# Kernel optimization log

Hardware: AMD Instinct MI355X
Metric: run time of the kernel (lower is better)

Reference implementation:

```python
import jax, jax.numpy as jnp
import numpy as np

H, KVH, D, R = 32, 8, 128, 32
MASK_OUT = 0.5
NEG = -1e9  # stand-in for finfo.min to avoid -inf accumulation; preserves ordering/softmax
ROPE_THETA = 10000.0


def _rope_tables(S, D):
    inv = 1.0 / (ROPE_THETA ** (np.arange(0, D, 2, dtype=np.float32) / D))
    t = np.arange(S, dtype=np.float32)
    freqs = np.outer(t, inv)
    emb = np.concatenate([freqs, freqs], axis=-1)  # [S, D]
    return jnp.asarray(np.cos(emb)), jnp.asarray(np.sin(emb))


def _apply_rope(x, cos, sin):
    # x: [B,H,S,D]; cos/sin: [S,D]
    x1, x2 = jnp.split(x, 2, axis=-1)
    rot = jnp.concatenate([-x2, x1], axis=-1)
    return x * cos[None, None] + rot * sin[None, None]


def setup_inputs() -> dict:
    B, S, E = 1, 1024, 4096
    key = jax.random.key(0)
    ks = jax.random.split(key, 9)
    n = lambda k, shp, sc=0.02: jax.random.normal(k, shp, jnp.float32) * sc
    return {
        'hidden_states': n(ks[0], (B, S, E), 1.0),
        'wq': n(ks[1], (E, H * D)),
        'wk': n(ks[2], (E, KVH * D)),
        'wv': n(ks[3], (E, KVH * D)),
        'wo': n(ks[4], (H * D, E)),
        'mixq': n(ks[5], (E, R)),
        'mixk': n(ks[6], (E, R)),
        'q_pos': n(ks[7], (S, H, R, D)),
        'k_pos': n(ks[8], (S, H, R, D)),
    }


def reference(hidden_states, wq, wk, wv, wo, mixq, mixk, q_pos, k_pos):
    B, S, E = hidden_states.shape
    rep = H // KVH
    # QKV projections -> [B, heads, S, D]
    q = (hidden_states @ wq).reshape(B, S, H, D).transpose(0, 2, 1, 3)
    k = (hidden_states @ wk).reshape(B, S, KVH, D).transpose(0, 2, 1, 3)
    v = (hidden_states @ wv).reshape(B, S, KVH, D).transpose(0, 2, 1, 3)
    k = jnp.repeat(k, rep, axis=1)  # repeat_kv (GQA expand) -> [B,H,S,D]
    v = jnp.repeat(v, rep, axis=1)

    cos, sin = _rope_tables(S, D)
    qr = _apply_rope(q, cos, sin)
    kr = _apply_rope(k, cos, sin)
    scale = 1.0 / jnp.sqrt(jnp.float32(D))
    true_score = jnp.einsum('bhqd,bhkd->bhqk', qr, kr) * scale  # [B,H,S,S]

    # low-rank position-dependent draft score
    lrq = hidden_states @ mixq  # [B,S,R]
    lrk = hidden_states @ mixk
    pq = jnp.einsum('bmr,mhrd->bhmd', lrq, q_pos)  # [B,H,S,D]
    pk = jnp.einsum('bnr,nhrd->bhnd', lrk, k_pos)
    draft_score = jnp.einsum('bhqd,bhkd->bhqk', pq, pk)  # [B,H,S,S]

    causal = jnp.where(jnp.tril(jnp.ones((S, S), dtype=bool)), 0.0, NEG).astype(jnp.float32)[None, None]
    draft_score = draft_score + causal  # prefill: add causal mask to draft score

    num_remain = S - int(S * MASK_OUT)
    _, draft_idx = jax.lax.top_k(draft_score, num_remain)  # [B,H,S,K]

    # scatter 0 at kept kv positions, NEG elsewhere
    bi = jnp.arange(B)[:, None, None, None]
    hi = jnp.arange(H)[None, :, None, None]
    qi = jnp.arange(S)[None, None, :, None]
    topk_mask = jnp.full((B, H, S, S), NEG, jnp.float32).at[bi, hi, qi, draft_idx].set(0.0)

    probs = jax.nn.softmax(true_score + causal + topk_mask, axis=-1)
    out = jnp.einsum('bhqk,bhkd->bqhd', probs, v).reshape(B, S, H * D)
    return out @ wo
```

## Files before the change

kernel.cpp:

```cpp
#include <hip/hip_runtime.h>
#include <hip/hip_bf16.h>
#include <math.h>


typedef unsigned short u16;
typedef unsigned long long u64;
using bf16x8 = __attribute__((ext_vector_type(8))) short;
using f32x4  = __attribute__((ext_vector_type(4))) float;

#define NEGBIG -1e30f
#define QSCALE 0.08838834764831845f

__device__ __forceinline__ unsigned int fkey(float f) {
    unsigned int u = __float_as_uint(f);
    return (u & 0x80000000u) ? ~u : (u | 0x80000000u);
}

__device__ __forceinline__ u16 f2b(float f) {
    union { float f; unsigned u; } x; x.f = f;
    unsigned r = x.u + 0x7fffu + ((x.u >> 16) & 1u);
    return (u16)(r >> 16);
}

__device__ __forceinline__ void gl_lds16(const u16* g, u16* l) {
    __builtin_amdgcn_global_load_lds(
        (__attribute__((address_space(1))) void*)(g),
        (__attribute__((address_space(3))) void*)(l), 16, 0, 0);
}

__device__ __forceinline__ void rope_table_calc(int row, int i,
    float* __restrict__ cosb, float* __restrict__ sinb)
{
    double inv = pow(10000.0, -((double)(2 * i)) / 128.0);
    double ang = (double)row * inv;
    cosb[row * 64 + i] = (float)cos(ang);
    sinb[row * 64 + i] = (float)sin(ang);
}

__device__ __forceinline__ void transpose_tile(
    const float* __restrict__ in, u16* __restrict__ out, int Kdim, int N,
    int bx, int by)
{
    __shared__ u16 tile[64][66];
    int n0 = bx * 64, k0 = by * 64;
    int t = threadIdx.x;
#pragma unroll
    for (int u = 0; u < 16; ++u) {
        int e = u * 256 + t; int r = e >> 6, c = e & 63;
        tile[r][c] = f2b(in[(size_t)(k0 + r) * N + n0 + c]);
    }
    __syncthreads();
#pragma unroll
    for (int u = 0; u < 16; ++u) {
        int e = u * 256 + t; int r = e >> 6, c = e & 63;
        out[(size_t)(n0 + r) * Kdim + k0 + c] = tile[c][r];
    }
}

__global__ __launch_bounds__(256) void transpose_bf16_kernel(
    const float* __restrict__ in, u16* __restrict__ out, int Kdim, int N)
{
    transpose_tile(in, out, Kdim, N, blockIdx.x, blockIdx.y);
}

__global__ __launch_bounds__(256) void init_kernel(
    const float* __restrict__ hs, u16* __restrict__ hs_bf,
    float* __restrict__ cosb, float* __restrict__ sinb)
{
    int bx = blockIdx.x, t = threadIdx.x;
    if (bx < 4096) {
        int i = bx * 256 + t;
        float4 v = ((const float4*)hs)[i];
        u16 o[4] = {f2b(v.x), f2b(v.y), f2b(v.z), f2b(v.w)};
        ((uint2*)hs_bf)[i] = *(const uint2*)o;
    } else {
        rope_table_calc((bx - 4096) * 4 + (t >> 6), t & 63, cosb, sinb);
    }
}

__global__ __launch_bounds__(256) void transpose_qkvw_kernel(
    const float* __restrict__ wq, const float* __restrict__ wk, const float* __restrict__ wv,
    u16* __restrict__ wqT, u16* __restrict__ wkT, u16* __restrict__ wvT)
{
    int bx = blockIdx.x;
    const float* in; u16* outp; int N;
    if (bx < 64)      { in = wq; outp = wqT; N = 4096; }
    else if (bx < 80) { in = wk; outp = wkT; N = 1024; bx -= 64; }
    else              { in = wv; outp = wvT; N = 1024; bx -= 80; }
    transpose_tile(in, outp, 4096, N, bx, blockIdx.y);
}

__global__ __launch_bounds__(128) void rope_pack2_kernel(
    const float* __restrict__ qb, const float* __restrict__ kb,
    const float* __restrict__ cosb, const float* __restrict__ sinb,
    u16* __restrict__ qr, u16* __restrict__ kr)
{
    int s = blockIdx.x, h = blockIdx.y, d = threadIdx.x;
    const float* src; u16* dst; int W; float scale;
    if (h < 32) { src = qb; dst = qr; W = 4096; scale = QSCALE; }
    else        { h -= 32; src = kb; dst = kr; W = 1024; scale = 1.0f; }
    float x  = src[(size_t)s * W + h * 128 + d];
    float x2 = src[(size_t)s * W + h * 128 + (d ^ 64)];
    float cs = cosb[s * 64 + (d & 63)];
    float sn = sinb[s * 64 + (d & 63)];
    float rot = (d < 64) ? -x2 : x2;
    dst[((size_t)h * 1024 + s) * 128 + d] = f2b((x * cs + rot * sn) * scale);
}

__global__ __launch_bounds__(256) void lr_kernel(
    const float* __restrict__ hs, const float* __restrict__ mixq, const float* __restrict__ mixk,
    float* __restrict__ lrq, float* __restrict__ lrk)
{
    __shared__ float row[4096];
    __shared__ float part[2][32][4];
    int m = blockIdx.x, t = threadIdx.x;
#pragma unroll
    for (int u = 0; u < 4; ++u)
        ((float4*)row)[t + u * 256] = ((const float4*)(hs + (size_t)m * 4096))[t + u * 256];
    __syncthreads();
    int r = t & 31, which = (t >> 5) & 1, quarter = t >> 6;
    const float* mix = which ? mixk : mixq;
    float acc = 0.f;
    int kbase = quarter * 1024;
#pragma unroll 8
    for (int kk = 0; kk < 1024; ++kk)
        acc = fmaf(row[kbase + kk], mix[(size_t)(kbase + kk) * 32 + r], acc);
    part[which][r][quarter] = acc;
    __syncthreads();
    if (t < 64) {
        int r2 = t & 31, w2 = t >> 5;
        float s = part[w2][r2][0] + part[w2][r2][1] + part[w2][r2][2] + part[w2][r2][3];
        (w2 ? lrk : lrq)[(size_t)m * 32 + r2] = s;
    }
}

__global__ __launch_bounds__(128) void ppos2_kernel(
    const float* __restrict__ lrq, const float* __restrict__ lrk,
    const float* __restrict__ qpos, const float* __restrict__ kpos,
    float* __restrict__ pq, float* __restrict__ pk)
{
    int h = blockIdx.x, by = blockIdx.y, d = threadIdx.x;
    const float* lr; const float* pos; float* outp; int m;
    if (by < 512) { m = 512 + by; lr = lrq; pos = qpos; outp = pq; }
    else          { m = by - 512; lr = lrk; pos = kpos; outp = pk; }
    __shared__ float lrs[32];
    if (d < 32) lrs[d] = lr[(size_t)m * 32 + d];
    __syncthreads();
    const float* base = pos + ((size_t)(m * 32 + h) * 32) * 128 + d;
    float acc = 0.f;
#pragma unroll
    for (int r = 0; r < 32; ++r)
        acc = fmaf(lrs[r], base[(size_t)r * 128], acc);
    outp[((size_t)h * 1024 + m) * 128 + d] = acc;
}

__global__ __launch_bounds__(256) void init_fused_kernel(
    const float* __restrict__ hs, u16* __restrict__ hs_bf,
    float* __restrict__ cosb, float* __restrict__ sinb,
    const float* __restrict__ mixq, const float* __restrict__ mixk,
    float* __restrict__ lrq, float* __restrict__ lrk,
    const float* __restrict__ wq, const float* __restrict__ wk, const float* __restrict__ wv,
    u16* __restrict__ wqT, u16* __restrict__ wkT, u16* __restrict__ wvT)
{
    __shared__ float row[4096];
    __shared__ float part[2][32][4];
    int bx = blockIdx.x, t = threadIdx.x;
    if (bx < 4096) {
        int i = bx * 256 + t;
        float4 v = ((const float4*)hs)[i];
        u16 o[4] = {f2b(v.x), f2b(v.y), f2b(v.z), f2b(v.w)};
        ((uint2*)hs_bf)[i] = *(const uint2*)o;
    } else if (bx < 4352) {
        rope_table_calc((bx - 4096) * 4 + (t >> 6), t & 63, cosb, sinb);
    } else if (bx < 5376) {
        int m = bx - 4352;
#pragma unroll
        for (int u = 0; u < 4; ++u)
            ((float4*)row)[t + u * 256] = ((const float4*)(hs + (size_t)m * 4096))[t + u * 256];
        __syncthreads();
        int r = t & 31, which = (t >> 5) & 1, quarter = t >> 6;
        const float* mix = which ? mixk : mixq;
        float acc = 0.f;
        int kbase = quarter * 1024;
#pragma unroll 8
        for (int kk = 0; kk < 1024; ++kk)
            acc = fmaf(row[kbase + kk], mix[(size_t)(kbase + kk) * 32 + r], acc);
        part[which][r][quarter] = acc;
        __syncthreads();
        if (t < 64) {
            int r2 = t & 31, w2 = t >> 5;
            float s = part[w2][r2][0] + part[w2][r2][1] + part[w2][r2][2] + part[w2][r2][3];
            (w2 ? lrk : lrq)[(size_t)m * 32 + r2] = s;
        }
    } else {
        int idx = bx - 5376;
        int bxT = idx % 96, byT = idx / 96;
        const float* in; u16* outp; int N;
        if (bxT < 64)      { in = wq; outp = wqT; N = 4096; }
        else if (bxT < 80) { in = wk; outp = wkT; N = 1024; bxT -= 64; }
        else               { in = wv; outp = wvT; N = 1024; bxT -= 80; }
        transpose_tile(in, outp, 4096, N, bxT, byT);
    }
}

__device__ __forceinline__ void gemm_bf16_panel(
    const u16* __restrict__ Ap, const u16* __restrict__ Bp,
    float* __restrict__ Cp, int Kdim, int kbase, int klen, int Cst)
{
    __shared__ u16 As[128 * 32];
    __shared__ u16 Bs[128 * 32];
    const int t = threadIdx.x;
    const int wave = t >> 6, lane = t & 63;
    const int wr = wave >> 1, wc = wave & 1;
    const int fr = lane & 15, fq = lane >> 4;

    f32x4 acc[4][4];
#pragma unroll
    for (int m = 0; m < 4; ++m)
#pragma unroll
        for (int n = 0; n < 4; ++n) acc[m][n] = 0.f;

    const int srow = 32 * wave + (lane >> 2);
    const int skc = (lane & 3) * 8;
    const u16* aS = Ap + (size_t)srow * Kdim + kbase + skc;
    const u16* bS = Bp + (size_t)srow * Kdim + kbase + skc;
    u16* aD0 = As + 1024 * wave;  u16* aD1 = aD0 + 512;
    u16* bD0 = Bs + 1024 * wave;  u16* bD1 = bD0 + 512;

    const int aoff = (wr * 64 + fr) * 32 + fq * 8;
    const int boff = (wc * 64 + fr) * 32 + fq * 8;

    for (int k0 = 0; k0 < klen; k0 += 32) {
        __syncthreads();
        gl_lds16(aS + k0, aD0);
        gl_lds16(aS + (size_t)16 * Kdim + k0, aD1);
        gl_lds16(bS + k0, bD0);
        gl_lds16(bS + (size_t)16 * Kdim + k0, bD1);
        __syncthreads();

        bf16x8 af[4], bfr[4];
#pragma unroll
        for (int m = 0; m < 4; ++m) af[m] = *(const bf16x8*)(As + aoff + m * 512);
#pragma unroll
        for (int n = 0; n < 4; ++n) bfr[n] = *(const bf16x8*)(Bs + boff + n * 512);
#pragma unroll
        for (int m = 0; m < 4; ++m)
#pragma unroll
            for (int n = 0; n < 4; ++n)
                acc[m][n] = __builtin_amdgcn_mfma_f32_16x16x32_bf16(af[m], bfr[n], acc[m][n], 0, 0, 0);
    }

    float* Cb = Cp + (size_t)(wr * 64 + fq * 4) * Cst + wc * 64 + fr;
#pragma unroll
    for (int m = 0; m < 4; ++m)
#pragma unroll
        for (int j = 0; j < 4; ++j)
#pragma unroll
            for (int n = 0; n < 4; ++n)
                Cb[(size_t)(m * 16 + j) * Cst + n * 16] = acc[m][n][j];
}

__global__ __launch_bounds__(256) void gemm_qkv_bf16_kernel(
    const u16* __restrict__ hs_bf, const u16* __restrict__ wqT,
    const u16* __restrict__ wkT, const u16* __restrict__ wvT,
    float* __restrict__ q, float* __restrict__ k, float* __restrict__ v)
{
    int bn = blockIdx.x, bm = blockIdx.y;
    const u16* Bsel; float* Csel; int Ncols;
    if (bn < 32)      { Bsel = wqT; Csel = q; Ncols = 4096; }
    else if (bn < 40) { Bsel = wkT; Csel = k; Ncols = 1024; bn -= 32; }
    else              { Bsel = wvT; Csel = v; Ncols = 1024; bn -= 40; }
    gemm_bf16_panel(hs_bf + (size_t)bm * 128 * 4096, Bsel + (size_t)bn * 128 * 4096,
                    Csel + (size_t)bm * 128 * Ncols + bn * 128, 4096, 0, 4096, Ncols);
}

__global__ __launch_bounds__(256) void gemm_wo_bf16_kernel(
    const u16* __restrict__ attn_bf, const u16* __restrict__ woT, float* __restrict__ out)
{
    int bn = blockIdx.x, bm = blockIdx.y;
    gemm_bf16_panel(attn_bf + (size_t)bm * 128 * 4096, woT + (size_t)bn * 128 * 4096,
                    out + (size_t)bm * 128 * 4096 + bn * 128, 4096, 0, 4096, 4096);
}

__global__ __launch_bounds__(256) void qkv_ppos_kernel(
    const u16* __restrict__ hs_bf, const u16* __restrict__ wqT,
    const u16* __restrict__ wkT, const u16* __restrict__ wvT,
    float* __restrict__ C,
    const float* __restrict__ lrq, const float* __restrict__ lrk,
    const float* __restrict__ qpos, const float* __restrict__ kpos,
    float* __restrict__ pq, float* __restrict__ pk)
{
    int bx = blockIdx.x, t = threadIdx.x;
    if (bx < 384) {
        int bn = bx % 48, bm = bx / 48;
        const u16* Bsel; int bnrow;
        if (bn < 32)      { Bsel = wqT; bnrow = bn; }
        else if (bn < 40) { Bsel = wkT; bnrow = bn - 32; }
        else              { Bsel = wvT; bnrow = bn - 40; }
        gemm_bf16_panel(hs_bf + (size_t)bm * 128 * 4096, Bsel + (size_t)bnrow * 128 * 4096,
                        C + (size_t)bm * 128 * 6144 + bn * 128, 4096, 0, 4096, 6144);
    } else {
        int idx = bx - 384;
        int bp = idx >> 5, h = idx & 31;
        int sub = t >> 7, d = t & 127;
        int by = bp * 2 + sub;
        const float* lr; const float* pos; float* outp; int m;
        if (by < 512) { m = 512 + by; lr = lrq; pos = qpos; outp = pq; }
        else          { m = by - 512; lr = lrk; pos = kpos; outp = pk; }
        __shared__ float lrs[2][32];
        if (d < 32) lrs[sub][d] = lr[(size_t)m * 32 + d];
        __syncthreads();
        const float* base = pos + ((size_t)(m * 32 + h) * 32) * 128 + d;
        float acc = 0.f;
#pragma unroll
        for (int r = 0; r < 32; ++r)
            acc = fmaf(lrs[sub][r], base[(size_t)r * 128], acc);
        outp[((size_t)h * 1024 + m) * 128 + d] = acc;
    }
}

__device__ __forceinline__ void reduce_rope_item(
    const float* __restrict__ C,
    const float* __restrict__ cosb, const float* __restrict__ sinb,
    u16* __restrict__ qr, u16* __restrict__ kr, int bx)
{
    int t = threadIdx.x;
    int sp = bx & 511, h40 = bx >> 9;
    int s = sp * 2 + (t >> 7), d = t & 127;
    int col; u16* dst; float scale;
    if (h40 < 32) { col = h40 * 128 + d; dst = qr + ((size_t)h40 * 1024 + s) * 128 + d; scale = QSCALE; }
    else { col = 4096 + (h40 - 32) * 128 + d; dst = kr + ((size_t)(h40 - 32) * 1024 + s) * 128 + d; scale = 1.0f; }
    int colp = col ^ 64;
    float x  = C[(size_t)s * 6144 + col];
    float x2 = C[(size_t)s * 6144 + colp];
    float cs = cosb[s * 64 + (d & 63)];
    float sn = sinb[s * 64 + (d & 63)];
    float rot = (d < 64) ? -x2 : x2;
    *dst = f2b((x * cs + rot * sn) * scale);
}

__device__ __forceinline__ void v_transpose_dev(
    const float* __restrict__ C, u16* __restrict__ vT, int idx)
{
    __shared__ u16 vtile[64][66];
    int bxT = idx & 15, byT = idx >> 4;
    int n0 = bxT * 64, k0 = byT * 64;
    int t = threadIdx.x;
#pragma unroll
    for (int u = 0; u < 16; ++u) {
        int e = u * 256 + t; int r = e >> 6, c = e & 63;
        vtile[r][c] = f2b(C[(size_t)(k0 + r) * 6144 + 5120 + n0 + c]);
    }
    __syncthreads();
#pragma unroll
    for (int u = 0; u < 16; ++u) {
        int e = u * 256 + t; int r = e >> 6, c = e & 63;
        vT[(size_t)(n0 + r) * 1024 + k0 + c] = vtile[c][r];
    }
}

__device__ __forceinline__ void draft_tile_compute(
    const float* __restrict__ pq, const float* __restrict__ pk,
    float* __restrict__ scores, int h0, int idx, int hh)
{
    int bm, bc;
    if (idx < 10)      { bm = 4; bc = idx; }
    else if (idx < 22) { bm = 5; bc = idx - 10; }
    else if (idx < 36) { bm = 6; bc = idx - 22; }
    else               { bm = 7; bc = idx - 36; }

    const float* A  = pq + ((size_t)(h0 + hh) * 1024 + bm * 128) * 128;
    const float* BT = pk + ((size_t)(h0 + hh) * 1024 + bc * 64) * 128;
    float* Cs = scores + ((size_t)hh * 512 + (bm - 4) * 128) * 1024 + bc * 64;

    __shared__ float As[8][128];
    __shared__ float Bs[8][64];
    const int t = threadIdx.x;
    const int tx = t & 15, ty = (t >> 4) & 15;

    float acc[8][4];
#pragma unroll
    for (int u = 0; u < 8; ++u)
#pragma unroll
        for (int w = 0; w < 4; ++w) acc[u][w] = 0.f;

    const int ai = t >> 1, ah = (t & 1) * 4;
    const int bi = t >> 2, bh = (t & 3) * 2;
    const float* Ap = A + (size_t)ai * 128 + ah;
    const float* Bp = BT + (size_t)bi * 128 + bh;

    for (int k0 = 0; k0 < 128; k0 += 8) {
        float4 av = *(const float4*)(Ap + k0);
        float2 bv = *(const float2*)(Bp + k0);
        __syncthreads();
        As[ah + 0][ai] = av.x; As[ah + 1][ai] = av.y;
        As[ah + 2][ai] = av.z; As[ah + 3][ai] = av.w;
        Bs[bh][bi] = bv.x; Bs[bh + 1][bi] = bv.y;
        __syncthreads();
#pragma unroll
        for (int kk = 0; kk < 8; ++kk) {
            float4 a0 = *(const float4*)(&As[kk][ty * 4]);
            float4 a1 = *(const float4*)(&As[kk][64 + ty * 4]);
            float4 b0 = *(const float4*)(&Bs[kk][tx * 4]);
            float aa[8] = {a0.x, a0.y, a0.z, a0.w, a1.x, a1.y, a1.z, a1.w};
#pragma unroll
            for (int u = 0; u < 8; ++u) {
                acc[u][0] = fmaf(aa[u], b0.x, acc[u][0]);
                acc[u][1] = fmaf(aa[u], b0.y, acc[u][1]);
                acc[u][2] = fmaf(aa[u], b0.z, acc[u][2]);
                acc[u][3] = fmaf(aa[u], b0.w, acc[u][3]);
            }
        }
    }
#pragma unroll
    for (int u = 0; u < 8; ++u) {
        int row = (u < 4) ? (ty * 4 + u) : (64 + ty * 4 + (u - 4));
        *(float4*)(Cs + (size_t)row * 1024 + tx * 4)
            = make_float4(acc[u][0], acc[u][1], acc[u][2], acc[u][3]);
    }
}

__global__ __launch_bounds__(256) void draft_gemm_kernel(
    const float* __restrict__ pq, const float* __restrict__ pk,
    float* __restrict__ scores, int h0)
{
    draft_tile_compute(pq, pk, scores, h0, blockIdx.x, blockIdx.y);
}

__global__ __launch_bounds__(256) void draft0_fused_kernel(
    const float* __restrict__ pq, const float* __restrict__ pk,
    float* __restrict__ scores, const float* __restrict__ C,
    const float* __restrict__ cosb, const float* __restrict__ sinb,
    u16* __restrict__ qr, u16* __restrict__ kr, u16* __restrict__ vT)
{
    int bx = blockIdx.x;
    if (bx < 416) draft_tile_compute(pq, pk, scores, 0, bx % 52, bx / 52);
    else if (bx < 416 + 20480) reduce_rope_item(C, cosb, sinb, qr, kr, bx - 416);
    else v_transpose_dev(C, vT, bx - 416 - 20480);
}

__global__ __launch_bounds__(256) void draft1_fused_kernel(
    const float* __restrict__ pq, const float* __restrict__ pk,
    float* __restrict__ scores, const float* __restrict__ wo, u16* __restrict__ woT)
{
    int bx = blockIdx.x;
    if (bx < 416) draft_tile_compute(pq, pk, scores, 8, bx % 52, bx / 52);
    else { int i = bx - 416; transpose_tile(wo, woT, 4096, 4096, i & 63, i >> 6); }
}

__global__ __launch_bounds__(256) void topk_select_kernel(
    const float* __restrict__ scores, int h0,
    unsigned long long* __restrict__ mask)
{
    int qt = blockIdx.x, hh = blockIdx.y;
    int h = h0 + hh;
    int t = threadIdx.x;
    const int i = t >> 4, jj = t & 15;
    const int lrow = qt * 16 + i;
    const int qrow = 512 + lrow;

    const float* src = scores + ((size_t)hh * 512 + lrow) * 1024;

    unsigned int vals[64];
#pragma unroll
    for (int g = 0; g < 16; ++g) {
        float4 v = *(const float4*)(src + g * 64 + jj * 4);
        int col = g * 64 + jj * 4;
        vals[g * 4 + 0] = fkey((col + 0) <= qrow ? v.x : NEGBIG);
        vals[g * 4 + 1] = fkey((col + 1) <= qrow ? v.y : NEGBIG);
        vals[g * 4 + 2] = fkey((col + 2) <= qrow ? v.z : NEGBIG);
        vals[g * 4 + 3] = fkey((col + 3) <= qrow ? v.w : NEGBIG);
    }

    unsigned int p = 0u;
    int kth = 512;
    for (int b = 31; b >= 0; --b) {
        unsigned int bit = 1u << b;
        unsigned int himask = (b == 31) ? 0u : (0xFFFFFFFFu << (b + 1));
        int cnt = 0;
#pragma unroll
        for (int n = 0; n < 64; ++n)
            cnt += (int)((((vals[n] ^ p) & himask) == 0u) && ((vals[n] & bit) != 0u));
        cnt += __shfl_xor(cnt, 1);
        cnt += __shfl_xor(cnt, 2);
        cnt += __shfl_xor(cnt, 4);
        cnt += __shfl_xor(cnt, 8);
        if (cnt >= kth) p |= bit; else kth -= cnt;
    }

    unsigned long long wpart[16];
#pragma unroll
    for (int w = 0; w < 16; ++w) wpart[w] = 0ull;
#pragma unroll
    for (int g = 0; g < 16; ++g)
#pragma unroll
        for (int e = 0; e < 4; ++e)
            wpart[g] |= ((unsigned long long)(vals[g * 4 + e] >= p)) << (4 * jj + e);
#pragma unroll
    for (int s = 1; s < 16; s <<= 1) {
#pragma unroll
        for (int w = 0; w < 16; ++w)
            wpart[w] |= __shfl_xor(wpart[w], s);
    }
    mask[((size_t)h * 1024 + qrow) * 16 + jj] = wpart[jj];
}

__global__ __launch_bounds__(256) void gemm_wo_sk_kernel(
    const u16* __restrict__ attn_bf, const u16* __restrict__ woT,
    float* __restrict__ D0, float* __restrict__ D1)
{
    int bn = blockIdx.x, bm = blockIdx.y, g = blockIdx.z;
    float* C = g ? D1 : D0;
    gemm_bf16_panel(attn_bf + (size_t)bm * 128 * 4096, woT + (size_t)bn * 128 * 4096,
                    C + (size_t)bm * 128 * 4096 + bn * 128, 4096, g * 2048, 2048, 4096);
}

__global__ __launch_bounds__(256) void reduce_out_kernel(
    const float* __restrict__ D0, const float* __restrict__ D1, float* __restrict__ out)
{
    int i = blockIdx.x * 256 + threadIdx.x;
    float4 a = ((const float4*)D0)[i];
    float4 b = ((const float4*)D1)[i];
    ((float4*)out)[i] = make_float4(a.x + b.x, a.y + b.y, a.z + b.z, a.w + b.w);
}

#define ATTN_KP 136
#define ATTN_VP 72

__global__ __launch_bounds__(256) void attn_mfma_kernel(
    const u16* __restrict__ qr, const u16* __restrict__ kr,
    const u16* __restrict__ vT,
    const unsigned long long* __restrict__ mask,
    u16* __restrict__ attn)
{
    int bx = blockIdx.x;
    int qt = (bx & 1) ? (bx >> 1) : (15 - (bx >> 1));
    int h = blockIdx.y;
    int kvh = h >> 2;
    int q0 = qt * 64;
    int t = threadIdx.x;
    int wave = t >> 6, lane = t & 63;
    int fr = lane & 15, fq = lane >> 4;
    int qrow = q0 + wave * 16 + fr;

    __shared__ u16 Ks[64 * ATTN_KP];
    __shared__ u16 Vs[128 * ATTN_VP];

    bf16x8 qf[4];
    const u16* qbase = qr + ((size_t)h * 1024 + qrow) * 128 + fq * 8;
#pragma unroll
    for (int kc = 0; kc < 4; ++kc)
        qf[kc] = *(const bf16x8*)(qbase + kc * 32);

    float m_run = -3.0e38f, l_run = 0.f;
    f32x4 accO[8];
#pragma unroll
    for (int m2 = 0; m2 < 8; ++m2) accO[m2] = 0.f;

    const unsigned long long* mrow = mask + ((size_t)h * 1024 + qrow) * 16;
    const bool use_mask = (qrow >= 512);
    const u16* kgh = kr + (size_t)kvh * 1024 * 128;
    const u16* vgh = vT + (size_t)kvh * 128 * 1024;

    int ntiles = qt + 1;
    for (int c = 0; c < ntiles; ++c) {
        int kv0 = c * 64;
        __syncthreads();
#pragma unroll
        for (int u = 0; u < 4; ++u) {
            int e = t + u * 256;
            int row = e >> 4, bc2 = (e & 15) * 8;
            uint4 d4 = *(const uint4*)(kgh + ((size_t)(kv0 + row)) * 128 + bc2);
            *(uint4*)(&Ks[row * ATTN_KP + bc2]) = d4;
        }
#pragma unroll
        for (int u = 0; u < 4; ++u) {
            int e = t + u * 256;
            int row = e >> 3, bc2 = (e & 7) * 8;
            uint4 d4 = *(const uint4*)(vgh + (size_t)row * 1024 + kv0 + bc2);
            *(uint4*)(&Vs[row * ATTN_VP + bc2]) = d4;
        }
        __syncthreads();

        f32x4 accS[4];
        accS[0] = 0.f; accS[1] = 0.f; accS[2] = 0.f; accS[3] = 0.f;
#pragma unroll
        for (int t2 = 0; t2 < 4; ++t2)
#pragma unroll
            for (int kc = 0; kc < 4; ++kc) {
                bf16x8 kf = *(const bf16x8*)(&Ks[(t2 * 16 + fr) * ATTN_KP + kc * 32 + fq * 8]);
                accS[t2] = __builtin_amdgcn_mfma_f32_16x16x32_bf16(kf, qf[kc], accS[t2], 0, 0, 0);
            }

        unsigned long long mw = use_mask ? mrow[c] : ~0ull;
        float p[4][4];
        float tmax = -3.0e38f;
#pragma unroll
        for (int t2 = 0; t2 < 4; ++t2)
#pragma unroll
            for (int j = 0; j < 4; ++j) {
                int kvi = (t2 << 4) + (fq << 2) + j;
                bool ok = ((mw >> kvi) & 1ull) && (kv0 + kvi <= qrow);
                float s = ok ? accS[t2][j] : -3.0e38f;
                p[t2][j] = s;
                tmax = fmaxf(tmax, s);
            }
        tmax = fmaxf(tmax, __shfl_xor(tmax, 16));
        tmax = fmaxf(tmax, __shfl_xor(tmax, 32));
        float m_new = fmaxf(m_run, tmax);
        float sf = __expf(m_run - m_new);
        float psum = 0.f;
#pragma unroll
        for (int t2 = 0; t2 < 4; ++t2)
#pragma unroll
            for (int j = 0; j < 4; ++j) {
                float e = (p[t2][j] > -1.0e38f) ? __expf(p[t2][j] - m_new) : 0.f;
                p[t2][j] = e;
                psum += e;
            }
        psum += __shfl_xor(psum, 16);
        psum += __shfl_xor(psum, 32);
        l_run = l_run * sf + psum;
        m_run = m_new;

#pragma unroll
        for (int m2 = 0; m2 < 8; ++m2) accO[m2] *= sf;

        union { uint4 u; bf16x8 b; } pc[2];
        int srcA = fr + ((fq & 1) << 5);
        int srcB = srcA + 16;
        bool hi = (fq & 2) != 0;
#pragma unroll
        for (int half = 0; half < 2; ++half) {
            unsigned W0, W1, W2, W3;
            asm("v_cvt_pk_bf16_f32 %0, %1, %2" : "=v"(W0) : "v"(p[2 * half][0]),     "v"(p[2 * half][1]));
            asm("v_cvt_pk_bf16_f32 %0, %1, %2" : "=v"(W1) : "v"(p[2 * half][2]),     "v"(p[2 * half][3]));
            asm("v_cvt_pk_bf16_f32 %0, %1, %2" : "=v"(W2) : "v"(p[2 * half + 1][0]), "v"(p[2 * half + 1][1]));
            asm("v_cvt_pk_bf16_f32 %0, %1, %2" : "=v"(W3) : "v"(p[2 * half + 1][2]), "v"(p[2 * half + 1][3]));
            unsigned a0 = __shfl(W0, srcA), a1 = __shfl(W1, srcA);
            unsigned a2 = __shfl(W2, srcA), a3 = __shfl(W3, srcA);
            unsigned b0 = __shfl(W0, srcB), b1 = __shfl(W1, srcB);
            unsigned b2 = __shfl(W2, srcB), b3 = __shfl(W3, srcB);
            pc[half].u.x = hi ? a2 : a0;
            pc[half].u.y = hi ? a3 : a1;
            pc[half].u.z = hi ? b2 : b0;
            pc[half].u.w = hi ? b3 : b1;
        }

#pragma unroll
        for (int m2 = 0; m2 < 8; ++m2) {
            bf16x8 vf0 = *(const bf16x8*)(&Vs[(m2 * 16 + fr) * ATTN_VP + fq * 8]);
            accO[m2] = __builtin_amdgcn_mfma_f32_16x16x32_bf16(vf0, pc[0].b, accO[m2], 0, 0, 0);
            bf16x8 vf1 = *(const bf16x8*)(&Vs[(m2 * 16 + fr) * ATTN_VP + 32 + fq * 8]);
            accO[m2] = __builtin_amdgcn_mfma_f32_16x16x32_bf16(vf1, pc[1].b, accO[m2], 0, 0, 0);
        }
    }

    float il = 1.0f / l_run;
    u16* obase = attn + (size_t)qrow * 4096 + h * 128 + fq * 4;
#pragma unroll
    for (int m2 = 0; m2 < 8; ++m2) {
        uint2 st;
        st.x = (unsigned)f2b(accO[m2][0] * il) | ((unsigned)f2b(accO[m2][1] * il) << 16);
        st.y = (unsigned)f2b(accO[m2][2] * il) | ((unsigned)f2b(accO[m2][3] * il) << 16);
        *(uint2*)(obase + m2 * 16) = st;
    }
}

extern "C" void kernel_launch(void* const* d_in, const int* in_sizes, int n_in,
                              void* d_out, int out_size, void* d_ws, size_t ws_size,
                              hipStream_t stream)
{
    (void)in_sizes; (void)n_in; (void)out_size;
    const float* hs   = (const float*)d_in[0];
    const float* wq   = (const float*)d_in[1];
    const float* wk   = (const float*)d_in[2];
    const float* wv   = (const float*)d_in[3];
    const float* wo   = (const float*)d_in[4];
    const float* mixq = (const float*)d_in[5];
    const float* mixk = (const float*)d_in[6];
    const float* qpos = (const float*)d_in[7];
    const float* kpos = (const float*)d_in[8];
    float* out = (float*)d_out;
    char* B = (char*)d_ws;
    const size_t MB = 1ull << 20;

    if (ws_size >= 123 * MB) {
        u16* hs_bf = (u16*)(B);
        u16* wkT   = (u16*)(B + 8 * MB);
        u16* wvT   = (u16*)(B + 16 * MB);
        u16* wqT   = (u16*)(B + 24 * MB);
        u16* qr    = (u16*)(B + 24 * MB);
        u16* kr    = (u16*)(B + 32 * MB);
        u16* vT    = (u16*)(B + 34 * MB);
        float* scores = (float*)(B + 36 * MB);
        u64* mask  = (u64*)(B + 52 * MB);
        float* C   = (float*)(B + 56 * MB);
        u16* woT   = (u16*)(B + 56 * MB);
        float* pq  = (float*)(B + 88 * MB);
        float* pk  = (float*)(B + 104 * MB);
        float* D0  = (float*)(B + 88 * MB);
        float* D1  = (float*)(B + 104 * MB);
        float* lrq = (float*)(B + 120 * MB);
        float* lrk = lrq + 32768;
        float* cosb = lrk + 32768;
        float* sinb = cosb + 65536;
        u16* attn_bf = hs_bf;

        hipLaunchKernelGGL(init_fused_kernel, dim3(11520), dim3(256), 0, stream,
                           hs, hs_bf, cosb, sinb, mixq, mixk, lrq, lrk,
                           wq, wk, wv, wqT, wkT, wvT);
        hipLaunchKernelGGL(qkv_ppos_kernel, dim3(24960), dim3(256), 0, stream,
                           hs_bf, wqT, wkT, wvT, C, lrq, lrk, qpos, kpos, pq, pk);
        hipLaunchKernelGGL(draft0_fused_kernel, dim3(21152), dim3(256), 0, stream,
                           pq, pk, scores, C, cosb, sinb, qr, kr, vT);
        hipLaunchKernelGGL(topk_select_kernel, dim3(32, 8), dim3(256), 0, stream,
                           scores, 0, mask);
        hipLaunchKernelGGL(draft1_fused_kernel, dim3(4512), dim3(256), 0, stream,
                           pq, pk, scores, wo, woT);
        hipLaunchKernelGGL(topk_select_kernel, dim3(32, 8), dim3(256), 0, stream,
                           scores, 8, mask);
        hipLaunchKernelGGL(draft_gemm_kernel, dim3(52, 8), dim3(256), 0, stream,
                           pq, pk, scores, 16);
        hipLaunchKernelGGL(topk_select_kernel, dim3(32, 8), dim3(256), 0, stream,
                           scores, 16, mask);
        hipLaunchKernelGGL(draft_gemm_kernel, dim3(52, 8), dim3(256), 0, stream,
                           pq, pk, scores, 24);
        hipLaunchKernelGGL(topk_select_kernel, dim3(32, 8), dim3(256), 0, stream,
                           scores, 24, mask);
        hipLaunchKernelGGL(attn_mfma_kernel, dim3(16, 32), dim3(256), 0, stream,
                           qr, kr, vT, mask, attn_bf);
        hipLaunchKernelGGL(gemm_wo_sk_kernel, dim3(32, 8, 2), dim3(256), 0, stream,
                           attn_bf, woT, D0, D1);
        hipLaunchKernelGGL(reduce_out_kernel, dim3(4096), dim3(256), 0, stream,
                           D0, D1, out);
    } else {
        float* ws   = (float*)d_ws;
        float* qb   = ws;
        float* kb   = qb + 4194304;
        float* vb   = kb + 1048576;
        float* pq   = vb + 1048576;
        float* pk   = pq + 4194304;
        float* lrq  = pk + 4194304;
        float* lrk  = lrq + 32768;
        float* cosb = lrk + 32768;
        float* sinb = cosb + 65536;
        u64* mask = (u64*)(sinb + 65536);
        u16* hs_bf = (u16*)(ws + 14876672 + 1048576);
        u16* wkT   = hs_bf + 4194304;
        u16* wvT   = wkT + 4194304;
        u16* wqT   = (u16*)pq;
        u16* woT   = (u16*)pq;
        u16* qr_bf = (u16*)pq;
        u16* kr_bf = (u16*)pk;
        u16* vT_bf = (u16*)(pk + 1048576);
        u16* attn_bf = hs_bf;
        float* scores = (float*)hs_bf;

        hipLaunchKernelGGL(init_kernel, dim3(4352), dim3(256), 0, stream, hs, hs_bf, cosb, sinb);
        hipLaunchKernelGGL(transpose_qkvw_kernel, dim3(96, 64), dim3(256), 0, stream,
                           wq, wk, wv, wqT, wkT, wvT);
        hipLaunchKernelGGL(gemm_qkv_bf16_kernel, dim3(48, 8), dim3(256), 0, stream,
                           hs_bf, wqT, wkT, wvT, qb, kb, vb);
        hipLaunchKernelGGL(lr_kernel, dim3(1024), dim3(256), 0, stream, hs, mixq, mixk, lrq, lrk);
        hipLaunchKernelGGL(ppos2_kernel, dim3(32, 1536), dim3(128), 0, stream,
                           lrq, lrk, qpos, kpos, pq, pk);
        for (int h0 = 0; h0 < 32; h0 += 8) {
            hipLaunchKernelGGL(draft_gemm_kernel, dim3(52, 8), dim3(256), 0, stream,
                               pq, pk, scores, h0);
            hipLaunchKernelGGL(topk_select_kernel, dim3(32, 8), dim3(256), 0, stream,
                               scores, h0, mask);
        }
        hipLaunchKernelGGL(rope_pack2_kernel, dim3(1024, 40), dim3(128), 0, stream,
                           qb, kb, cosb, sinb, qr_bf, kr_bf);
        hipLaunchKernelGGL(transpose_bf16_kernel, dim3(16, 16), dim3(256), 0, stream,
                           vb, vT_bf, 1024, 1024);
        hipLaunchKernelGGL(attn_mfma_kernel, dim3(16, 32), dim3(256), 0, stream,
                           qr_bf, kr_bf, vT_bf, mask, attn_bf);
        hipLaunchKernelGGL(transpose_bf16_kernel, dim3(64, 64), dim3(256), 0, stream,
                           wo, woT, 4096, 4096);
        hipLaunchKernelGGL(gemm_wo_bf16_kernel, dim3(32, 8), dim3(256), 0, stream,
                           attn_bf, woT, out);
    }
}
```

Measured before the change: 673.1 us.

## Overlap attention for first 16 heads with draft GEMM; split Wo GEMM three ways

Attention for heads 0-15, whose top-k masks are already available, now runs as extra blocks inside the kernel that computes the third group of draft scores. The final attention launch covers only heads 16-31. The output projection uses a three-way split-K into D0/D1/D2 with a three-input reduction, and D2 reuses the scores buffer after top-k has finished with it. This fills idle CUs and shortens the tail of the serial chain, at the cost of mixing heterogeneous blocks in one launch and an extra partial buffer to read in the reduction.

```diff
diff --git a/kernel.cpp b/kernel.cpp
--- a/kernel.cpp
+++ b/kernel.cpp
@@ -427,115 +427,16 @@
     draft_tile_compute(pq, pk, scores, h0, blockIdx.x, blockIdx.y);
 }
 
-__global__ __launch_bounds__(256) void draft0_fused_kernel(
-    const float* __restrict__ pq, const float* __restrict__ pk,
-    float* __restrict__ scores, const float* __restrict__ C,
-    const float* __restrict__ cosb, const float* __restrict__ sinb,
-    u16* __restrict__ qr, u16* __restrict__ kr, u16* __restrict__ vT)
-{
-    int bx = blockIdx.x;
-    if (bx < 416) draft_tile_compute(pq, pk, scores, 0, bx % 52, bx / 52);
-    else if (bx < 416 + 20480) reduce_rope_item(C, cosb, sinb, qr, kr, bx - 416);
-    else v_transpose_dev(C, vT, bx - 416 - 20480);
-}
-
-__global__ __launch_bounds__(256) void draft1_fused_kernel(
-    const float* __restrict__ pq, const float* __restrict__ pk,
-    float* __restrict__ scores, const float* __restrict__ wo, u16* __restrict__ woT)
-{
-    int bx = blockIdx.x;
-    if (bx < 416) draft_tile_compute(pq, pk, scores, 8, bx % 52, bx / 52);
-    else { int i = bx - 416; transpose_tile(wo, woT, 4096, 4096, i & 63, i >> 6); }
-}
-
-__global__ __launch_bounds__(256) void topk_select_kernel(
-    const float* __restrict__ scores, int h0,
-    unsigned long long* __restrict__ mask)
-{
-    int qt = blockIdx.x, hh = blockIdx.y;
-    int h = h0 + hh;
-    int t = threadIdx.x;
-    const int i = t >> 4, jj = t & 15;
-    const int lrow = qt * 16 + i;
-    const int qrow = 512 + lrow;
-
-    const float* src = scores + ((size_t)hh * 512 + lrow) * 1024;
-
-    unsigned int vals[64];
-#pragma unroll
-    for (int g = 0; g < 16; ++g) {
-        float4 v = *(const float4*)(src + g * 64 + jj * 4);
-        int col = g * 64 + jj * 4;
-        vals[g * 4 + 0] = fkey((col + 0) <= qrow ? v.x : NEGBIG);
-        vals[g * 4 + 1] = fkey((col + 1) <= qrow ? v.y : NEGBIG);
-        vals[g * 4 + 2] = fkey((col + 2) <= qrow ? v.z : NEGBIG);
-        vals[g * 4 + 3] = fkey((col + 3) <= qrow ? v.w : NEGBIG);
-    }
-
-    unsigned int p = 0u;
-    int kth = 512;
-    for (int b = 31; b >= 0; --b) {
-        unsigned int bit = 1u << b;
-        unsigned int himask = (b == 31) ? 0u : (0xFFFFFFFFu << (b + 1));
-        int cnt = 0;
-#pragma unroll
-        for (int n = 0; n < 64; ++n)
-            cnt += (int)((((vals[n] ^ p) & himask) == 0u) && ((vals[n] & bit) != 0u));
-        cnt += __shfl_xor(cnt, 1);
-        cnt += __shfl_xor(cnt, 2);
-        cnt += __shfl_xor(cnt, 4);
-        cnt += __shfl_xor(cnt, 8);
-        if (cnt >= kth) p |= bit; else kth -= cnt;
-    }
-
-    unsigned long long wpart[16];
-#pragma unroll
-    for (int w = 0; w < 16; ++w) wpart[w] = 0ull;
-#pragma unroll
-    for (int g = 0; g < 16; ++g)
-#pragma unroll
-        for (int e = 0; e < 4; ++e)
-            wpart[g] |= ((unsigned long long)(vals[g * 4 + e] >= p)) << (4 * jj + e);
-#pragma unroll
-    for (int s = 1; s < 16; s <<= 1) {
-#pragma unroll
-        for (int w = 0; w < 16; ++w)
-            wpart[w] |= __shfl_xor(wpart[w], s);
-    }
-    mask[((size_t)h * 1024 + qrow) * 16 + jj] = wpart[jj];
-}
-
-__global__ __launch_bounds__(256) void gemm_wo_sk_kernel(
-    const u16* __restrict__ attn_bf, const u16* __restrict__ woT,
-    float* __restrict__ D0, float* __restrict__ D1)
-{
-    int bn = blockIdx.x, bm = blockIdx.y, g = blockIdx.z;
-    float* C = g ? D1 : D0;
-    gemm_bf16_panel(attn_bf + (size_t)bm * 128 * 4096, woT + (size_t)bn * 128 * 4096,
-                    C + (size_t)bm * 128 * 4096 + bn * 128, 4096, g * 2048, 2048, 4096);
-}
-
-__global__ __launch_bounds__(256) void reduce_out_kernel(
-    const float* __restrict__ D0, const float* __restrict__ D1, float* __restrict__ out)
-{
-    int i = blockIdx.x * 256 + threadIdx.x;
-    float4 a = ((const float4*)D0)[i];
-    float4 b = ((const float4*)D1)[i];
-    ((float4*)out)[i] = make_float4(a.x + b.x, a.y + b.y, a.z + b.z, a.w + b.w);
-}
-
 #define ATTN_KP 136
 #define ATTN_VP 72
 
-__global__ __launch_bounds__(256) void attn_mfma_kernel(
+__device__ __forceinline__ void attn_block_compute(
     const u16* __restrict__ qr, const u16* __restrict__ kr,
     const u16* __restrict__ vT,
     const unsigned long long* __restrict__ mask,
-    u16* __restrict__ attn)
-{
-    int bx = blockIdx.x;
-    int qt = (bx & 1) ? (bx >> 1) : (15 - (bx >> 1));
-    int h = blockIdx.y;
+    u16* __restrict__ attn, int bxq, int h)
+{
+    int qt = (bxq & 1) ? (bxq >> 1) : (15 - (bxq >> 1));
     int kvh = h >> 2;
     int q0 = qt * 64;
     int t = threadIdx.x;
@@ -667,6 +568,132 @@
     }
 }
 
+__global__ __launch_bounds__(256) void attn_mfma_kernel(
+    const u16* __restrict__ qr, const u16* __restrict__ kr,
+    const u16* __restrict__ vT,
+    const unsigned long long* __restrict__ mask,
+    u16* __restrict__ attn, int hbase)
+{
+    attn_block_compute(qr, kr, vT, mask, attn, blockIdx.x, hbase + blockIdx.y);
+}
+
+__global__ __launch_bounds__(256) void draft0_fused_kernel(
+    const float* __restrict__ pq, const float* __restrict__ pk,
+    float* __restrict__ scores, const float* __restrict__ C,
+    const float* __restrict__ cosb, const float* __restrict__ sinb,
+    u16* __restrict__ qr, u16* __restrict__ kr, u16* __restrict__ vT)
+{
+    int bx = blockIdx.x;
+    if (bx < 416) draft_tile_compute(pq, pk, scores, 0, bx % 52, bx / 52);
+    else if (bx < 416 + 20480) reduce_rope_item(C, cosb, sinb, qr, kr, bx - 416);
+    else v_transpose_dev(C, vT, bx - 416 - 20480);
+}
+
+__global__ __launch_bounds__(256) void draft1_fused_kernel(
+    const float* __restrict__ pq, const float* __restrict__ pk,
+    float* __restrict__ scores, const float* __restrict__ wo, u16* __restrict__ woT)
+{
+    int bx = blockIdx.x;
+    if (bx < 416) draft_tile_compute(pq, pk, scores, 8, bx % 52, bx / 52);
+    else { int i = bx - 416; transpose_tile(wo, woT, 4096, 4096, i & 63, i >> 6); }
+}
+
+__global__ __launch_bounds__(256) void draft2_attn_kernel(
+    const float* __restrict__ pq, const float* __restrict__ pk,
+    float* __restrict__ scores,
+    const u16* __restrict__ qr, const u16* __restrict__ kr,
+    const u16* __restrict__ vT, const unsigned long long* __restrict__ mask,
+    u16* __restrict__ attn)
+{
+    int bx = blockIdx.x;
+    if (bx < 416) draft_tile_compute(pq, pk, scores, 16, bx % 52, bx / 52);
+    else {
+        int i = bx - 416;
+        attn_block_compute(qr, kr, vT, mask, attn, i & 15, i >> 4);
+    }
+}
+
+__global__ __launch_bounds__(256) void topk_select_kernel(
+    const float* __restrict__ scores, int h0,
+    unsigned long long* __restrict__ mask)
+{
+    int qt = blockIdx.x, hh = blockIdx.y;
+    int h = h0 + hh;
+    int t = threadIdx.x;
+    const int i = t >> 4, jj = t & 15;
+    const int lrow = qt * 16 + i;
+    const int qrow = 512 + lrow;
+
+    const float* src = scores + ((size_t)hh * 512 + lrow) * 1024;
+
+    unsigned int vals[64];
+#pragma unroll
+    for (int g = 0; g < 16; ++g) {
+        float4 v = *(const float4*)(src + g * 64 + jj * 4);
+        int col = g * 64 + jj * 4;
+        vals[g * 4 + 0] = fkey((col + 0) <= qrow ? v.x : NEGBIG);
+        vals[g * 4 + 1] = fkey((col + 1) <= qrow ? v.y : NEGBIG);
+        vals[g * 4 + 2] = fkey((col + 2) <= qrow ? v.z : NEGBIG);
+        vals[g * 4 + 3] = fkey((col + 3) <= qrow ? v.w : NEGBIG);
+    }
+
+    unsigned int p = 0u;
+    int kth = 512;
+    for (int b = 31; b >= 0; --b) {
+        unsigned int bit = 1u << b;
+        unsigned int himask = (b == 31) ? 0u : (0xFFFFFFFFu << (b + 1));
+        int cnt = 0;
+#pragma unroll
+        for (int n = 0; n < 64; ++n)
+            cnt += (int)((((vals[n] ^ p) & himask) == 0u) && ((vals[n] & bit) != 0u));
+        cnt += __shfl_xor(cnt, 1);
+        cnt += __shfl_xor(cnt, 2);
+        cnt += __shfl_xor(cnt, 4);
+        cnt += __shfl_xor(cnt, 8);
+        if (cnt >= kth) p |= bit; else kth -= cnt;
+    }
+
+    unsigned long long wpart[16];
+#pragma unroll
+    for (int w = 0; w < 16; ++w) wpart[w] = 0ull;
+#pragma unroll
+    for (int g = 0; g < 16; ++g)
+#pragma unroll
+        for (int e = 0; e < 4; ++e)
+            wpart[g] |= ((unsigned long long)(vals[g * 4 + e] >= p)) << (4 * jj + e);
+#pragma unroll
+    for (int s = 1; s < 16; s <<= 1) {
+#pragma unroll
+        for (int w = 0; w < 16; ++w)
+            wpart[w] |= __shfl_xor(wpart[w], s);
+    }
+    mask[((size_t)h * 1024 + qrow) * 16 + jj] = wpart[jj];
+}
+
+__global__ __launch_bounds__(256) void gemm_wo_sk3_kernel(
+    const u16* __restrict__ attn_bf, const u16* __restrict__ woT,
+    float* __restrict__ D0, float* __restrict__ D1, float* __restrict__ D2)
+{
+    int bn = blockIdx.x, bm = blockIdx.y, g = blockIdx.z;
+    float* C = (g == 0) ? D0 : (g == 1) ? D1 : D2;
+    int kbase = (g == 0) ? 0 : (g == 1) ? 1376 : 2752;
+    int klen  = (g == 2) ? 1344 : 1376;
+    gemm_bf16_panel(attn_bf + (size_t)bm * 128 * 4096, woT + (size_t)bn * 128 * 4096,
+                    C + (size_t)bm * 128 * 4096 + bn * 128, 4096, kbase, klen, 4096);
+}
+
+__global__ __launch_bounds__(256) void reduce_out3_kernel(
+    const float* __restrict__ D0, const float* __restrict__ D1,
+    const float* __restrict__ D2, float* __restrict__ out)
+{
+    int i = blockIdx.x * 256 + threadIdx.x;
+    float4 a = ((const float4*)D0)[i];
+    float4 b = ((const float4*)D1)[i];
+    float4 c = ((const float4*)D2)[i];
+    ((float4*)out)[i] = make_float4(a.x + b.x + c.x, a.y + b.y + c.y,
+                                    a.z + b.z + c.z, a.w + b.w + c.w);
+}
+
 extern "C" void kernel_launch(void* const* d_in, const int* in_sizes, int n_in,
                               void* d_out, int out_size, void* d_ws, size_t ws_size,
                               hipStream_t stream)
@@ -694,6 +721,7 @@
         u16* kr    = (u16*)(B + 32 * MB);
         u16* vT    = (u16*)(B + 34 * MB);
         float* scores = (float*)(B + 36 * MB);
+        float* D2  = (float*)(B + 36 * MB);
         u64* mask  = (u64*)(B + 52 * MB);
         float* C   = (float*)(B + 56 * MB);
         u16* woT   = (u16*)(B + 56 * MB);
@@ -720,20 +748,20 @@
                            pq, pk, scores, wo, woT);
         hipLaunchKernelGGL(topk_select_kernel, dim3(32, 8), dim3(256), 0, stream,
                            scores, 8, mask);
-        hipLaunchKernelGGL(draft_gemm_kernel, dim3(52, 8), dim3(256), 0, stream,
-                           pq, pk, scores, 16);
+        hipLaunchKernelGGL(draft2_attn_kernel, dim3(672), dim3(256), 0, stream,
+                           pq, pk, scores, qr, kr, vT, mask, attn_bf);
         hipLaunchKernelGGL(topk_select_kernel, dim3(32, 8), dim3(256), 0, stream,
                            scores, 16, mask);
         hipLaunchKernelGGL(draft_gemm_kernel, dim3(52, 8), dim3(256), 0, stream,
                            pq, pk, scores, 24);
         hipLaunchKernelGGL(topk_select_kernel, dim3(32, 8), dim3(256), 0, stream,
                            scores, 24, mask);
-        hipLaunchKernelGGL(attn_mfma_kernel, dim3(16, 32), dim3(256), 0, stream,
-                           qr, kr, vT, mask, attn_bf);
-        hipLaunchKernelGGL(gemm_wo_sk_kernel, dim3(32, 8, 2), dim3(256), 0, stream,
-                           attn_bf, woT, D0, D1);
-        hipLaunchKernelGGL(reduce_out_kernel, dim3(4096), dim3(256), 0, stream,
-                           D0, D1, out);
+        hipLaunchKernelGGL(attn_mfma_kernel, dim3(16, 16), dim3(256), 0, stream,
+                           qr, kr, vT, mask, attn_bf, 16);
+        hipLaunchKernelGGL(gemm_wo_sk3_kernel, dim3(32, 8, 3), dim3(256), 0, stream,
+                           attn_bf, woT, D0, D1, D2);
+        hipLaunchKernelGGL(reduce_out3_kernel, dim3(4096), dim3(256), 0, stream,
+                           D0, D1, D2, out);
     } else {
         float* ws   = (float*)d_ws;
         float* qb   = ws;
@@ -776,7 +804,7 @@
         hipLaunchKernelGGL(transpose_bf16_kernel, dim3(16, 16), dim3(256), 0, stream,
                            vb, vT_bf, 1024, 1024);
         hipLaunchKernelGGL(attn_mfma_kernel, dim3(16, 32), dim3(256), 0, stream,
-                           qr_bf, kr_bf, vT_bf, mask, attn_bf);
+                           qr_bf, kr_bf, vT_bf, mask, attn_bf, 0);
         hipLaunchKernelGGL(transpose_bf16_kernel, dim3(64, 64), dim3(256), 0, stream,
                            wo, woT, 4096, 4096);
         hipLaunchKernelGGL(gemm_wo_bf16_kernel, dim3(32, 8), dim3(256), 0, stream,
```

After: 723.4 us. 1.07x slower.
